# Optimization experiments

Measured on AMD Instinct MI355X. Metric: run time of the kernel, lower is better.

Reference implementation:

```python
import jax, jax.numpy as jnp
import numpy as np
from jax import lax

B, T, D = 16384, 60, 36   # n_traj, n_tp, n_dims
L, C, S = 10, 20, 9       # latent_dim, cluster_num, n_static
OUT = 8                   # mlp out (use_static=False)


def setup_inputs() -> dict:
    key = jax.random.key(0)
    ks = jax.random.split(key, 12)

    def w(k, shape):
        return jax.random.normal(k, shape, jnp.float32) / np.float32(np.sqrt(shape[0]))

    return {
        "data": jax.random.normal(ks[0], (B, T, D), jnp.float32),
        "time_steps": jnp.arange(T, dtype=jnp.float32),
        "static_data": jax.random.normal(ks[1], (B, S), jnp.float32),
        # GRU_unit_cluster gates: Linear(latent_dim + input_dim -> latent_dim)
        "W_update": w(ks[2], (L + D, L)), "b_update": jnp.zeros((L,), jnp.float32),
        "W_reset": w(ks[3], (L + D, L)), "b_reset": jnp.zeros((L,), jnp.float32),
        "W_new": w(ks[4], (L + D, L)), "b_new": jnp.zeros((L,), jnp.float32),
        # infer_emitter_z: Linear(latent_dim + cluster_num -> cluster_num)
        "W_emit": w(ks[5], (L + C, C)), "b_emit": jnp.zeros((C,), jnp.float32),
        # stand-in ODE func (z0_diffeq_solver.ode_func): tanh(Linear(latent->latent))
        "W_ode": w(ks[6], (L, L)), "b_ode": jnp.zeros((L,), jnp.float32),
        # final mlp: Linear(ts*10 + static -> 8)
        "W_mlp": w(ks[7], (T * L + S, OUT)), "b_mlp": jnp.zeros((OUT,), jnp.float32),
    }


def _forward(data, time_steps, static_data,
             W_update, b_update, W_reset, b_reset, W_new, b_new,
             W_emit, b_emit, W_ode, b_ode, W_mlp, b_mlp):
    n_traj = data.shape[0]
    # per-step dt: first step uses the synthetic 0.01 offset, then consecutive diffs
    dts = jnp.concatenate([jnp.full((1,), 0.01, time_steps.dtype), jnp.diff(time_steps)])
    xs = jnp.swapaxes(data, 0, 1)  # [T, B, D]

    def step(carry, inp):
        y_state, y_prob = carry        # [B, L], [B, C]
        x_t, dt = inp                  # [B, D], scalar
        # Euler step of the ODE between observations
        yi_ode = y_state + jnp.tanh(y_state @ W_ode + b_ode) * dt
        # GRU_unit_cluster update
        yc = jnp.concatenate([yi_ode, x_t], axis=-1)          # [B, L+D]
        u = jax.nn.sigmoid(yc @ W_update + b_update)
        r = jax.nn.sigmoid(yc @ W_reset + b_reset)
        cc = jnp.concatenate([yi_ode * r, x_t], axis=-1)
        new = cc @ W_new + b_new
        y_new = (1.0 - u) * new + u * yi_ode                  # [B, L]
        # emit_probs (concat_data=True path)
        zin = jnp.concatenate([y_prob, y_new], axis=-1)       # [B, C+L]
        y_prob_new = jax.nn.softmax(zin @ W_emit + b_emit, axis=-1)
        return (y_new, y_prob_new), y_new

    init = (jnp.zeros((n_traj, L), data.dtype), jnp.zeros((n_traj, C), data.dtype))
    _, states = lax.scan(step, init, (xs, dts))               # states: [T, B, L]

    vec = jnp.swapaxes(states, 0, 1).reshape(n_traj, T * L)   # [B, T*L]
    vec = jnp.concatenate([vec, static_data], axis=-1)        # [B, T*L + S]
    return vec @ W_mlp + b_mlp                                # [B, 8]


def reference(data, time_steps, static_data,
              W_update, b_update, W_reset, b_reset, W_new, b_new,
              W_emit, b_emit, W_ode, b_ode, W_mlp, b_mlp):
    return _forward(data, time_steps, static_data,
                    W_update, b_update, W_reset, b_reset, W_new, b_new,
                    W_emit, b_emit, W_ode, b_ode, W_mlp, b_mlp)
```

## Files before the change

### kernel.cpp

```cpp
#include <hip/hip_runtime.h>
#include <hip/hip_fp16.h>
#include <math.h>

#define B_TRAJ 16384
#define T_STEPS 60
#define D_IN 36
#define L_DIM 10
#define C_NUM 20
#define S_STAT 9
#define OUT_DIM 8
#define TT 2
#define NTILE (T_STEPS / TT)
#define XTS 1824
#define GSTRIDE 88

#define LOG2E 1.4426950408889634f

typedef float f32x2 __attribute__((ext_vector_type(2)));
__device__ __forceinline__ f32x2 pkfma(f32x2 a, f32x2 b, f32x2 c) {
    return __builtin_elementwise_fma(a, b, c);
}
__device__ __forceinline__ float rcp_fast(float x) { return __builtin_amdgcn_rcpf(x); }
__device__ __forceinline__ float exp2_fast(float x) { return __builtin_amdgcn_exp2f(x); }
__device__ __forceinline__ float sigm_fast(float x) {
    return rcp_fast(1.0f + exp2_fast(x * -LOG2E));
}
__device__ __forceinline__ float tanh_fast(float x) {
    const float t = fminf(fmaxf(x * (2.0f * LOG2E), -30.0f), 30.0f);
    return fmaf(-2.0f, rcp_fast(exp2_fast(t) + 1.0f), 1.0f);
}
#define WFENCE() __builtin_amdgcn_wave_barrier()

__global__ __launch_bounds__(64)
void dgm2_v9(
    const float* __restrict__ data,
    const float* __restrict__ time_steps,
    const float* __restrict__ static_data,
    const float* __restrict__ W_update,
    const float* __restrict__ b_update,
    const float* __restrict__ W_reset,
    const float* __restrict__ b_reset,
    const float* __restrict__ W_new,
    const float* __restrict__ b_new,
    const float* __restrict__ W_emit,
    const float* __restrict__ b_emit,
    const float* __restrict__ W_ode,
    const float* __restrict__ b_ode,
    const float* __restrict__ W_mlp,
    const float* __restrict__ b_mlp,
    float* __restrict__ out)
{
    __shared__ __align__(16) __half xprojH[4 * XTS];
    __shared__ __align__(16) float wbuf[4 * GSTRIDE];
    __shared__ float dts[T_STEPS];

    const int tid  = threadIdx.x;
    const int g    = tid >> 4;
    const int q    = tid & 15;
    const int traj = blockIdx.x * 4 + g;
    __half* xpj = xprojH + g * XTS;

    if (tid < T_STEPS) dts[tid] = (tid == 0) ? 0.01f : time_steps[tid] - time_steps[tid - 1];
    WFENCE();

    auto gate_ptr = [&](int c) -> const float* {
        return c < 10 ? W_update : (c < 20 ? W_reset : W_new);
    };
    auto gate_col = [&](int c) -> int { return c < 10 ? c : (c < 20 ? c - 10 : c - 20); };
    auto gate_bias = [&](int c) -> float {
        return c < 10 ? b_update[c] : (c < 20 ? b_reset[c - 10] : b_new[c - 20]);
    };

    {
        const int  c0   = q;
        const bool has1 = (q < 14);
        const int  c1   = has1 ? 16 + q : 29;
        const float* W0 = gate_ptr(c0); const int cc0 = gate_col(c0);
        const float* W1 = gate_ptr(c1); const int cc1 = gate_col(c1);

        f32x2 wxp0[18], wxp1[18];
#pragma unroll
        for (int j = 0; j < 18; ++j) {
            wxp0[j] = (f32x2){W0[(L_DIM + 2 * j) * L_DIM + cc0],
                              W0[(L_DIM + 2 * j + 1) * L_DIM + cc0]};
            const f32x2 v1 = (f32x2){W1[(L_DIM + 2 * j) * L_DIM + cc1],
                                     W1[(L_DIM + 2 * j + 1) * L_DIM + cc1]};
            wxp1[j] = has1 ? v1 : (f32x2){0.0f, 0.0f};
        }
        const float bcol0 = gate_bias(c0);
        const float bcol1 = has1 ? gate_bias(c1) : 0.0f;

        float* stagef = wbuf;
        const float* tb0 = data + (size_t)(blockIdx.x * 4) * (T_STEPS * D_IN);
        const int a_tr = tid / 18, a_rm = tid % 18, a_tt = a_rm / 9, a_c = a_rm % 9;
        const int bch = 64 + tid;
        const int b_tr = bch / 18, b_rm = bch % 18, b_tt = b_rm / 9, b_c = b_rm % 9;
        const bool hb = (tid < 8);

        {
            const float4 v0 = *reinterpret_cast<const float4*>(
                tb0 + (size_t)a_tr * (T_STEPS * D_IN) + a_tt * D_IN + a_c * 4);
            *reinterpret_cast<float4*>(stagef + (a_tr * TT + a_tt) * 36 + a_c * 4) = v0;
            if (hb) {
                const float4 v1 = *reinterpret_cast<const float4*>(
                    tb0 + (size_t)b_tr * (T_STEPS * D_IN) + b_tt * D_IN + b_c * 4);
                *reinterpret_cast<float4*>(stagef + (b_tr * TT + b_tt) * 36 + b_c * 4) = v1;
            }
        }
        WFENCE();

        for (int tile = 0; tile < NTILE; ++tile) {
            float4 pf0 = {}, pf1 = {};
            const bool more = (tile + 1 < NTILE);
            if (more) {
                pf0 = *reinterpret_cast<const float4*>(
                    tb0 + (size_t)a_tr * (T_STEPS * D_IN) + ((tile + 1) * TT + a_tt) * D_IN + a_c * 4);
                if (hb)
                    pf1 = *reinterpret_cast<const float4*>(
                        tb0 + (size_t)b_tr * (T_STEPS * D_IN) + ((tile + 1) * TT + b_tt) * D_IN + b_c * 4);
            }
#pragma unroll
            for (int tt = 0; tt < TT; ++tt) {
                const float* xrow = stagef + (g * TT + tt) * 36;
                f32x2 acc0 = (f32x2){bcol0, 0.0f};
                f32x2 acc1 = (f32x2){bcol1, 0.0f};
#pragma unroll
                for (int c = 0; c < 9; ++c) {
                    const float4 x4 = *reinterpret_cast<const float4*>(xrow + c * 4);
                    const f32x2 xlo = (f32x2){x4.x, x4.y};
                    const f32x2 xhi = (f32x2){x4.z, x4.w};
                    acc0 = pkfma(xlo, wxp0[2 * c], acc0);
                    acc0 = pkfma(xhi, wxp0[2 * c + 1], acc0);
                    acc1 = pkfma(xlo, wxp1[2 * c], acc1);
                    acc1 = pkfma(xhi, wxp1[2 * c + 1], acc1);
                }
                const int row = (tile * TT + tt) * 30;
                xpj[row + q] = __float2half(acc0.x + acc0.y);
                if (has1) xpj[row + 16 + q] = __float2half(acc1.x + acc1.y);
            }
            WFENCE();
            if (more) {
                *reinterpret_cast<float4*>(stagef + (a_tr * TT + a_tt) * 36 + a_c * 4) = pf0;
                if (hb)
                    *reinterpret_cast<float4*>(stagef + (b_tr * TT + b_tt) * 36 + b_c * 4) = pf1;
            }
            WFENCE();
        }
    }

    const bool qg = (q < 10);
    f32x2 wode2[5], wu2[5], wr2[5], wn2[5];
#pragma unroll
    for (int j = 0; j < 5; ++j) {
        if (qg) {
            wode2[j] = (f32x2){W_ode[(2 * j) * L_DIM + q], W_ode[(2 * j + 1) * L_DIM + q]};
            wu2[j]   = (f32x2){W_update[(2 * j) * L_DIM + q], W_update[(2 * j + 1) * L_DIM + q]};
            wr2[j]   = (f32x2){W_reset[(2 * j) * L_DIM + q], W_reset[(2 * j + 1) * L_DIM + q]};
            wn2[j]   = (f32x2){W_new[(2 * j) * L_DIM + q], W_new[(2 * j + 1) * L_DIM + q]};
        } else {
            wode2[j] = wu2[j] = wr2[j] = wn2[j] = (f32x2){0.0f, 0.0f};
        }
    }
    const float bode = qg ? b_ode[q] : 0.0f;

    const int  e0  = q;
    const bool he1 = (q < 4);
    const int  e1  = he1 ? 16 + q : 19;
    f32x2 wez0[10], wez1[10], wey0[5], wey1[5];
#pragma unroll
    for (int j = 0; j < 10; ++j) {
        wez0[j] = (f32x2){W_emit[(2 * j) * C_NUM + e0], W_emit[(2 * j + 1) * C_NUM + e0]};
        const f32x2 v1 = (f32x2){W_emit[(2 * j) * C_NUM + e1], W_emit[(2 * j + 1) * C_NUM + e1]};
        wez1[j] = he1 ? v1 : (f32x2){0.0f, 0.0f};
    }
#pragma unroll
    for (int j = 0; j < 5; ++j) {
        wey0[j] = (f32x2){W_emit[(C_NUM + 2 * j) * C_NUM + e0], W_emit[(C_NUM + 2 * j + 1) * C_NUM + e0]};
        const f32x2 v1 = (f32x2){W_emit[(C_NUM + 2 * j) * C_NUM + e1], W_emit[(C_NUM + 2 * j + 1) * C_NUM + e1]};
        wey1[j] = he1 ? v1 : (f32x2){0.0f, 0.0f};
    }
    const float be0 = b_emit[e0];
    const float be1 = he1 ? b_emit[e1] : 0.0f;

    float* grp = wbuf + g * GSTRIDE;
    float* gYI = grp;
    float* gYR = grp + 16;
    float* gY  = grp + 32;
    float* gZ  = grp + 48;

    auto ldvec = [&](const float* p, f32x2* d) {
        const float4 a = *reinterpret_cast<const float4*>(p);
        const float4 b = *reinterpret_cast<const float4*>(p + 4);
        const float2 c = *reinterpret_cast<const float2*>(p + 8);
        d[0] = (f32x2){a.x, a.y}; d[1] = (f32x2){a.z, a.w};
        d[2] = (f32x2){b.x, b.y}; d[3] = (f32x2){b.z, b.w};
        d[4] = (f32x2){c.x, c.y};
    };

    f32x2 y2[5];
#pragma unroll
    for (int k = 0; k < 5; ++k) y2[k] = (f32x2){0.0f, 0.0f};
    float yown = 0.0f;
    gZ[q] = 0.0f;
    if (he1) gZ[16 + q] = 0.0f;
    WFENCE();

    for (int t = 0; t < T_STEPS; ++t) {
        const float dt = dts[t];

        f32x2 g2 = (f32x2){bode, 0.0f};
#pragma unroll
        for (int k = 0; k < 5; ++k) g2 = pkfma(y2[k], wode2[k], g2);
        const float yis = fmaf(tanh_fast(g2.x + g2.y), dt, yown);
        gYI[q] = yis;
        WFENCE();
        f32x2 yi2[5];
        ldvec(gYI, yi2);

        const float xau = __half2float(xpj[t * 30 + q]);
        const float xar = __half2float(xpj[t * 30 + 10 + q]);
        const float xan = __half2float(xpj[t * 30 + 20 + q]);
        f32x2 au2 = (f32x2){xau, 0.0f};
        f32x2 ar2 = (f32x2){xar, 0.0f};
#pragma unroll
        for (int k = 0; k < 5; ++k) {
            au2 = pkfma(yi2[k], wu2[k], au2);
            ar2 = pkfma(yi2[k], wr2[k], ar2);
        }
        const float u = sigm_fast(au2.x + au2.y);
        const float r = sigm_fast(ar2.x + ar2.y);
        gYR[q] = r * yis;
        WFENCE();
        f32x2 yr2[5];
        ldvec(gYR, yr2);

        f32x2 an2 = (f32x2){xan, 0.0f};
#pragma unroll
        for (int k = 0; k < 5; ++k) an2 = pkfma(yr2[k], wn2[k], an2);
        const float nv = an2.x + an2.y;
        const float yn = fmaf(u, yis - nv, nv);
        yown = yn;
        gY[q] = yn;
        xpj[t * 30 + q] = __float2half(yn);
        WFENCE();
        ldvec(gY, y2);

        f32x2 zz[10];
        {
            const float4 z0 = *reinterpret_cast<const float4*>(gZ);
            const float4 z1 = *reinterpret_cast<const float4*>(gZ + 4);
            const float4 z2 = *reinterpret_cast<const float4*>(gZ + 8);
            const float4 z3 = *reinterpret_cast<const float4*>(gZ + 12);
            const float4 z4 = *reinterpret_cast<const float4*>(gZ + 16);
            zz[0] = (f32x2){z0.x, z0.y}; zz[1] = (f32x2){z0.z, z0.w};
            zz[2] = (f32x2){z1.x, z1.y}; zz[3] = (f32x2){z1.z, z1.w};
            zz[4] = (f32x2){z2.x, z2.y}; zz[5] = (f32x2){z2.z, z2.w};
            zz[6] = (f32x2){z3.x, z3.y}; zz[7] = (f32x2){z3.z, z3.w};
            zz[8] = (f32x2){z4.x, z4.y}; zz[9] = (f32x2){z4.z, z4.w};
        }
        f32x2 zd0 = (f32x2){0.0f, 0.0f}, zd1 = (f32x2){0.0f, 0.0f};
        f32x2 zs2 = (f32x2){0.0f, 0.0f};
#pragma unroll
        for (int j = 0; j < 10; ++j) {
            zd0 = pkfma(zz[j], wez0[j], zd0);
            zd1 = pkfma(zz[j], wez1[j], zd1);
            zs2 = zs2 + zz[j];
        }
        const float zsum = zs2.x + zs2.y;
        const float pinv = (t == 0) ? 0.0f : rcp_fast(zsum);
        f32x2 ev0 = (f32x2){fmaf(zd0.x + zd0.y, pinv, be0), 0.0f};
        f32x2 ev1 = (f32x2){fmaf(zd1.x + zd1.y, pinv, be1), 0.0f};
#pragma unroll
        for (int k = 0; k < 5; ++k) {
            ev0 = pkfma(y2[k], wey0[k], ev0);
            ev1 = pkfma(y2[k], wey1[k], ev1);
        }
        const float zv0 = exp2_fast(fminf((ev0.x + ev0.y) * LOG2E, 86.0f));
        const float zv1 = exp2_fast(fminf((ev1.x + ev1.y) * LOG2E, 86.0f));
        gZ[q] = zv0;
        if (he1) gZ[16 + q] = zv1;
    }

    WFENCE();
    {
        const int col = q & 7, tg = q >> 3;
        f32x2 o2 = (f32x2){0.0f, 0.0f};
        for (int tb = 0; tb < 30; ++tb) {
            const int t = tb * 2 + tg;
            const __half2* yh = reinterpret_cast<const __half2*>(xpj + t * 30);
            const float* wrow = W_mlp + (size_t)t * L_DIM * OUT_DIM + col;
#pragma unroll
            for (int q4 = 0; q4 < 5; ++q4) {
                const float2 yv = __half22float2(yh[q4]);
                const f32x2 w2 = (f32x2){wrow[(2 * q4) * OUT_DIM], wrow[(2 * q4 + 1) * OUT_DIM]};
                o2 = pkfma((f32x2){yv.x, yv.y}, w2, o2);
            }
        }
        float o8 = o2.x + o2.y;
        o8 += __shfl_xor(o8, 8, 16);
        if (q < OUT_DIM) {
            const float* stp = static_data + (size_t)traj * S_STAT;
            const float* wms = W_mlp + (size_t)(T_STEPS * L_DIM) * OUT_DIM;
#pragma unroll
            for (int i = 0; i < S_STAT; ++i) o8 += stp[i] * wms[i * OUT_DIM + q];
            out[(size_t)traj * OUT_DIM + q] = o8 + b_mlp[q];
        }
    }
}

extern "C" void kernel_launch(void* const* d_in, const int* in_sizes, int n_in,
                              void* d_out, int out_size, void* d_ws, size_t ws_size,
                              hipStream_t stream) {
    const float* data        = (const float*)d_in[0];
    const float* time_steps  = (const float*)d_in[1];
    const float* static_data = (const float*)d_in[2];
    const float* W_update    = (const float*)d_in[3];
    const float* b_update    = (const float*)d_in[4];
    const float* W_reset     = (const float*)d_in[5];
    const float* b_reset     = (const float*)d_in[6];
    const float* W_new       = (const float*)d_in[7];
    const float* b_new       = (const float*)d_in[8];
    const float* W_emit      = (const float*)d_in[9];
    const float* b_emit      = (const float*)d_in[10];
    const float* W_ode       = (const float*)d_in[11];
    const float* b_ode       = (const float*)d_in[12];
    const float* W_mlp       = (const float*)d_in[13];
    const float* b_mlp       = (const float*)d_in[14];
    float* out = (float*)d_out;

    dim3 grid(B_TRAJ / 4), block(64);
    hipLaunchKernelGGL(dgm2_v9, grid, block, 0, stream,
                       data, time_steps, static_data,
                       W_update, b_update, W_reset, b_reset, W_new, b_new,
                       W_emit, b_emit, W_ode, b_ode, W_mlp, b_mlp, out);
}
```

Baseline: 332.3 us.

## Restructure into 256-thread blocks with chunked x-projection, recurrence and head

```diff
diff --git a/kernel.cpp b/kernel.cpp
--- a/kernel.cpp
+++ b/kernel.cpp
@@ -9,10 +9,10 @@
 #define C_NUM 20
 #define S_STAT 9
 #define OUT_DIM 8
-#define TT 2
-#define NTILE (T_STEPS / TT)
-#define XTS 1824
-#define GSTRIDE 88
+#define CH 12
+#define NCHUNK 5
+#define NG 16
+#define SCS 72
 
 #define LOG2E 1.4426950408889634f
 
@@ -31,8 +31,8 @@
 }
 #define WFENCE() __builtin_amdgcn_wave_barrier()
 
-__global__ __launch_bounds__(64)
-void dgm2_v9(
+__global__ __launch_bounds__(256, 4)
+void dgm2_v10(
     const float* __restrict__ data,
     const float* __restrict__ time_steps,
     const float* __restrict__ static_data,
@@ -50,34 +50,43 @@
     const float* __restrict__ b_mlp,
     float* __restrict__ out)
 {
-    __shared__ __align__(16) __half xprojH[4 * XTS];
-    __shared__ __align__(16) float wbuf[4 * GSTRIDE];
-    __shared__ float dts[T_STEPS];
+    __shared__ __align__(16) __half xb[CH * NG * 16 * 4];
+    __shared__ __align__(16) __half yb[CH * NG * 10];
+    __shared__ __align__(16) float  sc[NG * SCS];
 
     const int tid  = threadIdx.x;
     const int g    = tid >> 4;
     const int q    = tid & 15;
-    const int traj = blockIdx.x * 4 + g;
-    __half* xpj = xprojH + g * XTS;
-
-    if (tid < T_STEPS) dts[tid] = (tid == 0) ? 0.01f : time_steps[tid] - time_steps[tid - 1];
-    WFENCE();
-
-    auto gate_ptr = [&](int c) -> const float* {
-        return c < 10 ? W_update : (c < 20 ? W_reset : W_new);
-    };
-    auto gate_col = [&](int c) -> int { return c < 10 ? c : (c < 20 ? c - 10 : c - 20); };
-    auto gate_bias = [&](int c) -> float {
-        return c < 10 ? b_update[c] : (c < 20 ? b_reset[c - 10] : b_new[c - 20]);
-    };
-
-    {
+    const int traj = blockIdx.x * NG + g;
+
+    const bool qg = (q < 10);
+    const int  qc = qg ? q : 0;
+
+    float* gYI = sc + g * SCS;
+    float* gYR = gYI + 16;
+    float* gY  = gYI + 32;
+    float* gZ  = gYI + 48;
+
+    f32x2 y2[5];
+#pragma unroll
+    for (int k = 0; k < 5; ++k) y2[k] = (f32x2){0.0f, 0.0f};
+    float yown = 0.0f;
+    f32x2 p2[4];
+#pragma unroll
+    for (int j = 0; j < 4; ++j) p2[j] = (f32x2){0.0f, 0.0f};
+    gZ[q] = 0.0f;
+    if (q < 4) gZ[16 + q] = 0.0f;
+
+    auto do_xproj = [&](int c) {
         const int  c0   = q;
         const bool has1 = (q < 14);
         const int  c1   = has1 ? 16 + q : 29;
-        const float* W0 = gate_ptr(c0); const int cc0 = gate_col(c0);
-        const float* W1 = gate_ptr(c1); const int cc1 = gate_col(c1);
-
+        const float* W0 = (c0 < 10) ? W_update : W_reset;
+        const int   cc0 = (c0 < 10) ? c0 : c0 - 10;
+        const int   gt0 = (c0 < 10) ? 0 : 1;
+        const float* W1 = (c1 < 20) ? W_reset : W_new;
+        const int   cc1 = (c1 < 20) ? c1 - 10 : c1 - 20;
+        const int   gt1 = (c1 < 20) ? 1 : 2;
         f32x2 wxp0[18], wxp1[18];
 #pragma unroll
         for (int j = 0; j < 18; ++j) {
@@ -87,106 +96,46 @@
                                      W1[(L_DIM + 2 * j + 1) * L_DIM + cc1]};
             wxp1[j] = has1 ? v1 : (f32x2){0.0f, 0.0f};
         }
-        const float bcol0 = gate_bias(c0);
-        const float bcol1 = has1 ? gate_bias(c1) : 0.0f;
-
-        float* stagef = wbuf;
-        const float* tb0 = data + (size_t)(blockIdx.x * 4) * (T_STEPS * D_IN);
-        const int a_tr = tid / 18, a_rm = tid % 18, a_tt = a_rm / 9, a_c = a_rm % 9;
-        const int bch = 64 + tid;
-        const int b_tr = bch / 18, b_rm = bch % 18, b_tt = b_rm / 9, b_c = b_rm % 9;
-        const bool hb = (tid < 8);
-
-        {
-            const float4 v0 = *reinterpret_cast<const float4*>(
-                tb0 + (size_t)a_tr * (T_STEPS * D_IN) + a_tt * D_IN + a_c * 4);
-            *reinterpret_cast<float4*>(stagef + (a_tr * TT + a_tt) * 36 + a_c * 4) = v0;
-            if (hb) {
-                const float4 v1 = *reinterpret_cast<const float4*>(
-                    tb0 + (size_t)b_tr * (T_STEPS * D_IN) + b_tt * D_IN + b_c * 4);
-                *reinterpret_cast<float4*>(stagef + (b_tr * TT + b_tt) * 36 + b_c * 4) = v1;
-            }
-        }
-        WFENCE();
-
-        for (int tile = 0; tile < NTILE; ++tile) {
-            float4 pf0 = {}, pf1 = {};
-            const bool more = (tile + 1 < NTILE);
-            if (more) {
-                pf0 = *reinterpret_cast<const float4*>(
-                    tb0 + (size_t)a_tr * (T_STEPS * D_IN) + ((tile + 1) * TT + a_tt) * D_IN + a_c * 4);
-                if (hb)
-                    pf1 = *reinterpret_cast<const float4*>(
-                        tb0 + (size_t)b_tr * (T_STEPS * D_IN) + ((tile + 1) * TT + b_tt) * D_IN + b_c * 4);
-            }
-#pragma unroll
-            for (int tt = 0; tt < TT; ++tt) {
-                const float* xrow = stagef + (g * TT + tt) * 36;
-                f32x2 acc0 = (f32x2){bcol0, 0.0f};
-                f32x2 acc1 = (f32x2){bcol1, 0.0f};
-#pragma unroll
-                for (int c = 0; c < 9; ++c) {
-                    const float4 x4 = *reinterpret_cast<const float4*>(xrow + c * 4);
-                    const f32x2 xlo = (f32x2){x4.x, x4.y};
-                    const f32x2 xhi = (f32x2){x4.z, x4.w};
-                    acc0 = pkfma(xlo, wxp0[2 * c], acc0);
-                    acc0 = pkfma(xhi, wxp0[2 * c + 1], acc0);
-                    acc1 = pkfma(xlo, wxp1[2 * c], acc1);
-                    acc1 = pkfma(xhi, wxp1[2 * c + 1], acc1);
+        const float b0 = (c0 < 10) ? b_update[c0] : b_reset[c0 - 10];
+        const float b1 = has1 ? ((c1 < 20) ? b_reset[c1 - 10] : b_new[c1 - 20]) : 0.0f;
+        const float* xbase = data + ((size_t)traj * T_STEPS + c * CH) * D_IN;
+        for (int tt = 0; tt < CH; ++tt) {
+            const float* xr = xbase + tt * D_IN;
+            f32x2 a0 = (f32x2){b0, 0.0f}, a1 = (f32x2){b1, 0.0f};
+#pragma unroll
+            for (int cq = 0; cq < 9; ++cq) {
+                const float4 x4 = *reinterpret_cast<const float4*>(xr + cq * 4);
+                const f32x2 xlo = (f32x2){x4.x, x4.y};
+                const f32x2 xhi = (f32x2){x4.z, x4.w};
+                a0 = pkfma(xlo, wxp0[2 * cq], a0);
+                a0 = pkfma(xhi, wxp0[2 * cq + 1], a0);
+                a1 = pkfma(xlo, wxp1[2 * cq], a1);
+                a1 = pkfma(xhi, wxp1[2 * cq + 1], a1);
+            }
+            __half* dst = xb + (size_t)((tt * NG + g) * 16) * 4;
+            dst[cc0 * 4 + gt0] = __float2half(a0.x + a0.y);
+            if (has1) dst[cc1 * 4 + gt1] = __float2half(a1.x + a1.y);
+        }
+    };
+
+    auto do_head = [&](int c) {
+        if (q < CH) {
+            const int t = c * CH + q;
+            const __half2* yrow = reinterpret_cast<const __half2*>(yb + (q * NG + g) * 10);
+            const float* wr = W_mlp + (size_t)t * (L_DIM * OUT_DIM);
+#pragma unroll
+            for (int k2 = 0; k2 < 5; ++k2) {
+                const float2 yv = __half22float2(yrow[k2]);
+                const float* w0 = wr + (2 * k2) * OUT_DIM;
+                const float* w1 = wr + (2 * k2 + 1) * OUT_DIM;
+#pragma unroll
+                for (int j = 0; j < 4; ++j) {
+                    p2[j] = pkfma((f32x2){yv.x, yv.x}, (f32x2){w0[2 * j], w0[2 * j + 1]}, p2[j]);
+                    p2[j] = pkfma((f32x2){yv.y, yv.y}, (f32x2){w1[2 * j], w1[2 * j + 1]}, p2[j]);
                 }
-                const int row = (tile * TT + tt) * 30;
-                xpj[row + q] = __float2half(acc0.x + acc0.y);
-                if (has1) xpj[row + 16 + q] = __float2half(acc1.x + acc1.y);
-            }
-            WFENCE();
-            if (more) {
-                *reinterpret_cast<float4*>(stagef + (a_tr * TT + a_tt) * 36 + a_c * 4) = pf0;
-                if (hb)
-                    *reinterpret_cast<float4*>(stagef + (b_tr * TT + b_tt) * 36 + b_c * 4) = pf1;
-            }
-            WFENCE();
-        }
-    }
-
-    const bool qg = (q < 10);
-    f32x2 wode2[5], wu2[5], wr2[5], wn2[5];
-#pragma unroll
-    for (int j = 0; j < 5; ++j) {
-        if (qg) {
-            wode2[j] = (f32x2){W_ode[(2 * j) * L_DIM + q], W_ode[(2 * j + 1) * L_DIM + q]};
-            wu2[j]   = (f32x2){W_update[(2 * j) * L_DIM + q], W_update[(2 * j + 1) * L_DIM + q]};
-            wr2[j]   = (f32x2){W_reset[(2 * j) * L_DIM + q], W_reset[(2 * j + 1) * L_DIM + q]};
-            wn2[j]   = (f32x2){W_new[(2 * j) * L_DIM + q], W_new[(2 * j + 1) * L_DIM + q]};
-        } else {
-            wode2[j] = wu2[j] = wr2[j] = wn2[j] = (f32x2){0.0f, 0.0f};
-        }
-    }
-    const float bode = qg ? b_ode[q] : 0.0f;
-
-    const int  e0  = q;
-    const bool he1 = (q < 4);
-    const int  e1  = he1 ? 16 + q : 19;
-    f32x2 wez0[10], wez1[10], wey0[5], wey1[5];
-#pragma unroll
-    for (int j = 0; j < 10; ++j) {
-        wez0[j] = (f32x2){W_emit[(2 * j) * C_NUM + e0], W_emit[(2 * j + 1) * C_NUM + e0]};
-        const f32x2 v1 = (f32x2){W_emit[(2 * j) * C_NUM + e1], W_emit[(2 * j + 1) * C_NUM + e1]};
-        wez1[j] = he1 ? v1 : (f32x2){0.0f, 0.0f};
-    }
-#pragma unroll
-    for (int j = 0; j < 5; ++j) {
-        wey0[j] = (f32x2){W_emit[(C_NUM + 2 * j) * C_NUM + e0], W_emit[(C_NUM + 2 * j + 1) * C_NUM + e0]};
-        const f32x2 v1 = (f32x2){W_emit[(C_NUM + 2 * j) * C_NUM + e1], W_emit[(C_NUM + 2 * j + 1) * C_NUM + e1]};
-        wey1[j] = he1 ? v1 : (f32x2){0.0f, 0.0f};
-    }
-    const float be0 = b_emit[e0];
-    const float be1 = he1 ? b_emit[e1] : 0.0f;
-
-    float* grp = wbuf + g * GSTRIDE;
-    float* gYI = grp;
-    float* gYR = grp + 16;
-    float* gY  = grp + 32;
-    float* gZ  = grp + 48;
+            }
+        }
+    };
 
     auto ldvec = [&](const float* p, f32x2* d) {
         const float4 a = *reinterpret_cast<const float4*>(p);
@@ -197,114 +146,147 @@
         d[4] = (f32x2){c.x, c.y};
     };
 
-    f32x2 y2[5];
-#pragma unroll
-    for (int k = 0; k < 5; ++k) y2[k] = (f32x2){0.0f, 0.0f};
-    float yown = 0.0f;
-    gZ[q] = 0.0f;
-    if (he1) gZ[16 + q] = 0.0f;
-    WFENCE();
-
-    for (int t = 0; t < T_STEPS; ++t) {
-        const float dt = dts[t];
-
-        f32x2 g2 = (f32x2){bode, 0.0f};
-#pragma unroll
-        for (int k = 0; k < 5; ++k) g2 = pkfma(y2[k], wode2[k], g2);
-        const float yis = fmaf(tanh_fast(g2.x + g2.y), dt, yown);
-        gYI[q] = yis;
-        WFENCE();
-        f32x2 yi2[5];
-        ldvec(gYI, yi2);
-
-        const float xau = __half2float(xpj[t * 30 + q]);
-        const float xar = __half2float(xpj[t * 30 + 10 + q]);
-        const float xan = __half2float(xpj[t * 30 + 20 + q]);
-        f32x2 au2 = (f32x2){xau, 0.0f};
-        f32x2 ar2 = (f32x2){xar, 0.0f};
-#pragma unroll
-        for (int k = 0; k < 5; ++k) {
-            au2 = pkfma(yi2[k], wu2[k], au2);
-            ar2 = pkfma(yi2[k], wr2[k], ar2);
-        }
-        const float u = sigm_fast(au2.x + au2.y);
-        const float r = sigm_fast(ar2.x + ar2.y);
-        gYR[q] = r * yis;
-        WFENCE();
-        f32x2 yr2[5];
-        ldvec(gYR, yr2);
-
-        f32x2 an2 = (f32x2){xan, 0.0f};
-#pragma unroll
-        for (int k = 0; k < 5; ++k) an2 = pkfma(yr2[k], wn2[k], an2);
-        const float nv = an2.x + an2.y;
-        const float yn = fmaf(u, yis - nv, nv);
-        yown = yn;
-        gY[q] = yn;
-        xpj[t * 30 + q] = __float2half(yn);
-        WFENCE();
-        ldvec(gY, y2);
-
-        f32x2 zz[10];
-        {
-            const float4 z0 = *reinterpret_cast<const float4*>(gZ);
-            const float4 z1 = *reinterpret_cast<const float4*>(gZ + 4);
-            const float4 z2 = *reinterpret_cast<const float4*>(gZ + 8);
-            const float4 z3 = *reinterpret_cast<const float4*>(gZ + 12);
-            const float4 z4 = *reinterpret_cast<const float4*>(gZ + 16);
-            zz[0] = (f32x2){z0.x, z0.y}; zz[1] = (f32x2){z0.z, z0.w};
-            zz[2] = (f32x2){z1.x, z1.y}; zz[3] = (f32x2){z1.z, z1.w};
-            zz[4] = (f32x2){z2.x, z2.y}; zz[5] = (f32x2){z2.z, z2.w};
-            zz[6] = (f32x2){z3.x, z3.y}; zz[7] = (f32x2){z3.z, z3.w};
-            zz[8] = (f32x2){z4.x, z4.y}; zz[9] = (f32x2){z4.z, z4.w};
-        }
-        f32x2 zd0 = (f32x2){0.0f, 0.0f}, zd1 = (f32x2){0.0f, 0.0f};
-        f32x2 zs2 = (f32x2){0.0f, 0.0f};
+    do_xproj(0);
+    __syncthreads();
+
+    for (int c = 0; c < NCHUNK; ++c) {
+        f32x2 wode2[5], wu2[5], wr2[5], wn2[5];
+#pragma unroll
+        for (int j = 0; j < 5; ++j) {
+            if (qg) {
+                wode2[j] = (f32x2){W_ode[(2 * j) * L_DIM + q], W_ode[(2 * j + 1) * L_DIM + q]};
+                wu2[j]   = (f32x2){W_update[(2 * j) * L_DIM + q], W_update[(2 * j + 1) * L_DIM + q]};
+                wr2[j]   = (f32x2){W_reset[(2 * j) * L_DIM + q], W_reset[(2 * j + 1) * L_DIM + q]};
+                wn2[j]   = (f32x2){W_new[(2 * j) * L_DIM + q], W_new[(2 * j + 1) * L_DIM + q]};
+            } else {
+                wode2[j] = wu2[j] = wr2[j] = wn2[j] = (f32x2){0.0f, 0.0f};
+            }
+        }
+        const float bode = qg ? b_ode[q] : 0.0f;
+        const int  e0  = q;
+        const bool he1 = (q < 4);
+        const int  e1  = he1 ? 16 + q : 19;
+        f32x2 wez0[10], wez1[10], wey0[5], wey1[5];
 #pragma unroll
         for (int j = 0; j < 10; ++j) {
-            zd0 = pkfma(zz[j], wez0[j], zd0);
-            zd1 = pkfma(zz[j], wez1[j], zd1);
-            zs2 = zs2 + zz[j];
-        }
-        const float zsum = zs2.x + zs2.y;
-        const float pinv = (t == 0) ? 0.0f : rcp_fast(zsum);
-        f32x2 ev0 = (f32x2){fmaf(zd0.x + zd0.y, pinv, be0), 0.0f};
-        f32x2 ev1 = (f32x2){fmaf(zd1.x + zd1.y, pinv, be1), 0.0f};
-#pragma unroll
-        for (int k = 0; k < 5; ++k) {
-            ev0 = pkfma(y2[k], wey0[k], ev0);
-            ev1 = pkfma(y2[k], wey1[k], ev1);
-        }
-        const float zv0 = exp2_fast(fminf((ev0.x + ev0.y) * LOG2E, 86.0f));
-        const float zv1 = exp2_fast(fminf((ev1.x + ev1.y) * LOG2E, 86.0f));
-        gZ[q] = zv0;
-        if (he1) gZ[16 + q] = zv1;
+            wez0[j] = (f32x2){W_emit[(2 * j) * C_NUM + e0], W_emit[(2 * j + 1) * C_NUM + e0]};
+            const f32x2 v1 = (f32x2){W_emit[(2 * j) * C_NUM + e1], W_emit[(2 * j + 1) * C_NUM + e1]};
+            wez1[j] = he1 ? v1 : (f32x2){0.0f, 0.0f};
+        }
+#pragma unroll
+        for (int j = 0; j < 5; ++j) {
+            wey0[j] = (f32x2){W_emit[(C_NUM + 2 * j) * C_NUM + e0],
+                              W_emit[(C_NUM + 2 * j + 1) * C_NUM + e0]};
+            const f32x2 v1 = (f32x2){W_emit[(C_NUM + 2 * j) * C_NUM + e1],
+                                     W_emit[(C_NUM + 2 * j + 1) * C_NUM + e1]};
+            wey1[j] = he1 ? v1 : (f32x2){0.0f, 0.0f};
+        }
+        const float be0 = b_emit[e0];
+        const float be1 = he1 ? b_emit[e1] : 0.0f;
+
+        for (int tt = 0; tt < CH; ++tt) {
+            const int t = c * CH + tt;
+            const float dt = (t == 0) ? 0.01f : time_steps[t] - time_steps[t - 1];
+
+            f32x2 g2 = (f32x2){bode, 0.0f};
+#pragma unroll
+            for (int k = 0; k < 5; ++k) g2 = pkfma(y2[k], wode2[k], g2);
+            const float yis = fmaf(tanh_fast(g2.x + g2.y), dt, yown);
+            gYI[q] = yis;
+            WFENCE();
+            f32x2 yi2[5];
+            ldvec(gYI, yi2);
+
+            union { float2 f2; __half2 h2[2]; } xu;
+            xu.f2 = *reinterpret_cast<const float2*>(xb + (size_t)((tt * NG + g) * 16 + qc) * 4);
+            const float2 xg0 = __half22float2(xu.h2[0]);
+            const float2 xg1 = __half22float2(xu.h2[1]);
+            const float xau = xg0.x, xar = xg0.y, xan = xg1.x;
+
+            f32x2 au2 = (f32x2){xau, 0.0f};
+            f32x2 ar2 = (f32x2){xar, 0.0f};
+#pragma unroll
+            for (int k = 0; k < 5; ++k) {
+                au2 = pkfma(yi2[k], wu2[k], au2);
+                ar2 = pkfma(yi2[k], wr2[k], ar2);
+            }
+            const float u = sigm_fast(au2.x + au2.y);
+            const float r = sigm_fast(ar2.x + ar2.y);
+            gYR[q] = r * yis;
+            WFENCE();
+            f32x2 yr2[5];
+            ldvec(gYR, yr2);
+
+            f32x2 an2 = (f32x2){xan, 0.0f};
+#pragma unroll
+            for (int k = 0; k < 5; ++k) an2 = pkfma(yr2[k], wn2[k], an2);
+            const float nv = an2.x + an2.y;
+            const float yn = fmaf(u, yis - nv, nv);
+            yown = yn;
+            gY[q] = yn;
+            if (qg) yb[(tt * NG + g) * 10 + q] = __float2half(yn);
+            WFENCE();
+            ldvec(gY, y2);
+
+            f32x2 zz[10];
+            {
+                const float4 z0 = *reinterpret_cast<const float4*>(gZ);
+                const float4 z1 = *reinterpret_cast<const float4*>(gZ + 4);
+                const float4 z2 = *reinterpret_cast<const float4*>(gZ + 8);
+                const float4 z3 = *reinterpret_cast<const float4*>(gZ + 12);
+                const float4 z4 = *reinterpret_cast<const float4*>(gZ + 16);
+                zz[0] = (f32x2){z0.x, z0.y}; zz[1] = (f32x2){z0.z, z0.w};
+                zz[2] = (f32x2){z1.x, z1.y}; zz[3] = (f32x2){z1.z, z1.w};
+                zz[4] = (f32x2){z2.x, z2.y}; zz[5] = (f32x2){z2.z, z2.w};
+                zz[6] = (f32x2){z3.x, z3.y}; zz[7] = (f32x2){z3.z, z3.w};
+                zz[8] = (f32x2){z4.x, z4.y}; zz[9] = (f32x2){z4.z, z4.w};
+            }
+            f32x2 zd0 = (f32x2){0.0f, 0.0f}, zd1 = (f32x2){0.0f, 0.0f};
+            f32x2 zs2 = (f32x2){0.0f, 0.0f};
+#pragma unroll
+            for (int j = 0; j < 10; ++j) {
+                zd0 = pkfma(zz[j], wez0[j], zd0);
+                zd1 = pkfma(zz[j], wez1[j], zd1);
+                zs2 = zs2 + zz[j];
+            }
+            const float zsum = zs2.x + zs2.y;
+            const float pinv = (t == 0) ? 0.0f : rcp_fast(zsum);
+            f32x2 ev0 = (f32x2){fmaf(zd0.x + zd0.y, pinv, be0), 0.0f};
+            f32x2 ev1 = (f32x2){fmaf(zd1.x + zd1.y, pinv, be1), 0.0f};
+#pragma unroll
+            for (int k = 0; k < 5; ++k) {
+                ev0 = pkfma(y2[k], wey0[k], ev0);
+                ev1 = pkfma(y2[k], wey1[k], ev1);
+            }
+            const float zv0 = exp2_fast(fminf((ev0.x + ev0.y) * LOG2E, 86.0f));
+            const float zv1 = exp2_fast(fminf((ev1.x + ev1.y) * LOG2E, 86.0f));
+            gZ[q] = zv0;
+            if (he1) gZ[16 + q] = zv1;
+        }
+
+        __syncthreads();
+        do_head(c);
+        if (c + 1 < NCHUNK) do_xproj(c + 1);
+        __syncthreads();
     }
 
-    WFENCE();
-    {
-        const int col = q & 7, tg = q >> 3;
-        f32x2 o2 = (f32x2){0.0f, 0.0f};
-        for (int tb = 0; tb < 30; ++tb) {
-            const int t = tb * 2 + tg;
-            const __half2* yh = reinterpret_cast<const __half2*>(xpj + t * 30);
-            const float* wrow = W_mlp + (size_t)t * L_DIM * OUT_DIM + col;
-#pragma unroll
-            for (int q4 = 0; q4 < 5; ++q4) {
-                const float2 yv = __half22float2(yh[q4]);
-                const f32x2 w2 = (f32x2){wrow[(2 * q4) * OUT_DIM], wrow[(2 * q4 + 1) * OUT_DIM]};
-                o2 = pkfma((f32x2){yv.x, yv.y}, w2, o2);
-            }
-        }
-        float o8 = o2.x + o2.y;
-        o8 += __shfl_xor(o8, 8, 16);
-        if (q < OUT_DIM) {
-            const float* stp = static_data + (size_t)traj * S_STAT;
-            const float* wms = W_mlp + (size_t)(T_STEPS * L_DIM) * OUT_DIM;
-#pragma unroll
-            for (int i = 0; i < S_STAT; ++i) o8 += stp[i] * wms[i * OUT_DIM + q];
-            out[(size_t)traj * OUT_DIM + q] = o8 + b_mlp[q];
-        }
+    float* wred = reinterpret_cast<float*>(xb);
+    if (q < CH) {
+        float* d = wred + (size_t)(g * CH + q) * 8;
+        *reinterpret_cast<f32x2*>(d + 0) = p2[0];
+        *reinterpret_cast<f32x2*>(d + 2) = p2[1];
+        *reinterpret_cast<f32x2*>(d + 4) = p2[2];
+        *reinterpret_cast<f32x2*>(d + 6) = p2[3];
+    }
+    __syncthreads();
+    if (q < OUT_DIM) {
+        float o = 0.0f;
+        for (int r = 0; r < CH; ++r) o += wred[(size_t)(g * CH + r) * 8 + q];
+        const float* stp = static_data + (size_t)traj * S_STAT;
+        const float* wms = W_mlp + (size_t)(T_STEPS * L_DIM) * OUT_DIM;
+#pragma unroll
+        for (int i = 0; i < S_STAT; ++i) o += stp[i] * wms[i * OUT_DIM + q];
+        out[(size_t)traj * OUT_DIM + q] = o + b_mlp[q];
     }
 }
 
@@ -328,8 +310,8 @@
     const float* b_mlp       = (const float*)d_in[14];
     float* out = (float*)d_out;
 
-    dim3 grid(B_TRAJ / 4), block(64);
-    hipLaunchKernelGGL(dgm2_v9, grid, block, 0, stream,
+    dim3 grid(B_TRAJ / NG), block(256);
+    hipLaunchKernelGGL(dgm2_v10, grid, block, 0, stream,
                        data, time_steps, static_data,
                        W_update, b_update, W_reset, b_reset, W_new, b_new,
                        W_emit, b_emit, W_ode, b_ode, W_mlp, b_mlp, out);
```

Result: slower. 738.5 us (+122.2%).
